# Optimization experiments

Hardware: AMD Instinct MI355X
Metric: run time of the kernel (lower is better)

Reference implementation:

```python
import jax, jax.numpy as jnp
import numpy as np

N, E, D = 50000, 1600000, 64


def setup_inputs() -> dict:
    key = jax.random.key(0)
    ks = jax.random.split(key, 10)
    s = 1.0 / np.sqrt(D)
    return {
        "x": jax.random.normal(ks[0], (N, D), dtype=jnp.float32),
        "edge_index": jax.random.randint(ks[1], (2, E), 0, N, dtype=jnp.int64),
        "edge_weight": jax.random.uniform(ks[2], (E,), dtype=jnp.float32),
        "W_rel1": jax.random.uniform(ks[3], (D, D), jnp.float32, -s, s),
        "b_rel1": jax.random.uniform(ks[4], (D,), jnp.float32, -s, s),
        "W_root1": jax.random.uniform(ks[5], (D, D), jnp.float32, -s, s),
        "W_rel2": jax.random.uniform(ks[6], (D, D), jnp.float32, -s, s),
        "b_rel2": jax.random.uniform(ks[7], (D,), jnp.float32, -s, s),
        "W_root2": jax.random.uniform(ks[8], (D, D), jnp.float32, -s, s),
    }


def graph_conv(x, src, dst, edge_weight, W_rel, b_rel, W_root):
    # message: edge_weight * x[src]; aggregate: sum into dst
    msg = edge_weight[:, None] * x[src]                      # [E, D]
    agg = jax.ops.segment_sum(msg, dst, num_segments=x.shape[0])  # [N, D]
    return agg @ W_rel.T + b_rel + x @ W_root.T


def reference(x, edge_index, edge_weight, W_rel1, b_rel1, W_root1, W_rel2, b_rel2, W_root2):
    src, dst = edge_index[0], edge_index[1]
    h = jax.nn.relu(graph_conv(x, src, dst, edge_weight, W_rel1, b_rel1, W_root1))
    # dropout is identity in eval mode
    h = jax.nn.relu(graph_conv(h, src, dst, edge_weight, W_rel2, b_rel2, W_root2))
    return h
```

## Files before the change

### kernel.cpp

```cpp
#include <hip/hip_runtime.h>


#define NN 50000
#define DD 64
#define EE 1600000
#define NPB 64
#define NB  ((NN + NPB - 1) / NPB)
#define PAD 2560
#define CHUNK 8192
#define NC ((EE + CHUNK - 1) / CHUNK)

static_assert(NC <= 256, "colscan_kernel scan width must cover all chunks");
static_assert(NB <= 1024, "LDS cursor arrays sized for NB");

typedef __attribute__((ext_vector_type(8))) short short8;
typedef __attribute__((ext_vector_type(4))) float f32x4;

__device__ __forceinline__ unsigned short f2bf(float f) {
    unsigned u = __float_as_uint(f);
    u += 0x7FFF + ((u >> 16) & 1);
    return (unsigned short)(u >> 16);
}
__device__ __forceinline__ float bflo(unsigned u) {
    return __uint_as_float(u << 16);
}
__device__ __forceinline__ float bfhi(unsigned u) {
    return __uint_as_float(u & 0xFFFF0000u);
}
__device__ __forceinline__ unsigned char f2fp8(float f) {
    unsigned p = __builtin_amdgcn_cvt_pk_fp8_f32(f, f, 0, false);
    return (unsigned char)(p & 0xFF);
}

#define XS_STR 72
#define WS_STR 72

template <typename TIn>
__device__ __forceinline__ void transform_body(
    int blk, int t,
    const TIn* __restrict__ xin,
    const float* __restrict__ Wrel, const float* __restrict__ Wroot,
    const float* __restrict__ bias,
    unsigned char* __restrict__ Z8, unsigned short* __restrict__ Yb,
    unsigned short* Xs, unsigned short* Ws)
{
    const int node0 = blk * 64;

#pragma unroll
    for (int i = 0; i < 8; ++i) {
        int flat = i * 256 + t;
        int row  = flat >> 4;
        int c4   = flat & 15;
        const float* src = (row < 64 ? Wrel + row * 64
                                     : Wroot + (row - 64) * 64) + c4 * 4;
        float4 v = *(const float4*)src;
        unsigned short* d = &Ws[row * WS_STR + c4 * 4];
        d[0] = f2bf(v.x); d[1] = f2bf(v.y); d[2] = f2bf(v.z); d[3] = f2bf(v.w);
    }
    if constexpr (sizeof(TIn) == 4) {
#pragma unroll
        for (int i = 0; i < 4; ++i) {
            int flat = i * 256 + t;
            int row  = flat >> 4;
            int c4   = flat & 15;
            int node = node0 + row;
            float4 v = make_float4(0.f, 0.f, 0.f, 0.f);
            if (node < NN) v = *(const float4*)((const float*)xin + (size_t)node * 64 + c4 * 4);
            unsigned short* d = &Xs[row * XS_STR + c4 * 4];
            d[0] = f2bf(v.x); d[1] = f2bf(v.y); d[2] = f2bf(v.z); d[3] = f2bf(v.w);
        }
    } else {
#pragma unroll
        for (int i = 0; i < 2; ++i) {
            int flat = i * 256 + t;
            int row  = flat >> 3;
            int c8   = flat & 7;
            int node = node0 + row;
            short8 v = {0,0,0,0,0,0,0,0};
            if (node < NN)
                v = *(const short8*)((const unsigned short*)xin + (size_t)node * 64 + c8 * 8);
            *(short8*)&Xs[row * XS_STR + c8 * 8] = v;
        }
    }
    __syncthreads();

    const int w    = t >> 6;
    const int lane = t & 63;
    const int l15  = lane & 15;
    const int quad = lane >> 4;

    short8 a0 = *(const short8*)&Xs[(w * 16 + l15) * XS_STR + quad * 8];
    short8 a1 = *(const short8*)&Xs[(w * 16 + l15) * XS_STR + 32 + quad * 8];

#pragma unroll
    for (int f = 0; f < 8; ++f) {
        short8 b0 = *(const short8*)&Ws[(f * 16 + l15) * WS_STR + quad * 8];
        short8 b1 = *(const short8*)&Ws[(f * 16 + l15) * WS_STR + 32 + quad * 8];
        f32x4 acc = {0.f, 0.f, 0.f, 0.f};
        acc = __builtin_amdgcn_mfma_f32_16x16x32_bf16(a0, b0, acc, 0, 0, 0);
        acc = __builtin_amdgcn_mfma_f32_16x16x32_bf16(a1, b1, acc, 0, 0, 0);
        const int col = f * 16 + l15;
#pragma unroll
        for (int r = 0; r < 4; ++r) {
            int node = node0 + w * 16 + quad * 4 + r;
            if (node < NN) {
                if (col < 64) Z8[(size_t)node * 64 + col] = f2fp8(acc[r]);
                else          Yb[(size_t)node * 64 + (col - 64)] =
                                  f2bf(acc[r] + bias[col - 64]);
            }
        }
    }
}

__global__ __launch_bounds__(256) void hist_t1_kernel(
    const int* __restrict__ ei, int* __restrict__ hist,
    const float* __restrict__ x,
    const float* __restrict__ Wrel, const float* __restrict__ Wroot,
    const float* __restrict__ bias,
    unsigned char* __restrict__ Z8, unsigned short* __restrict__ Yb)
{
    __shared__ int lh[NB];
    __shared__ unsigned short Xs[64 * XS_STR];
    __shared__ unsigned short Ws[128 * WS_STR];
    const int t = threadIdx.x;

    if (blockIdx.x < NC) {
        const int c = blockIdx.x;
        for (int b = t; b < NB; b += 256) lh[b] = 0;
        __syncthreads();
        const int base = c * CHUNK;
#pragma unroll 4
        for (int i = 0; i < CHUNK; i += 256) {
            int e = base + i + t;
            if (e < EE) atomicAdd(&lh[ei[EE + e] >> 6], 1);
        }
        __syncthreads();
        for (int b = t; b < NB; b += 256) hist[c * NB + b] = lh[b];
    } else {
        transform_body<float>(blockIdx.x - NC, t, x, Wrel, Wroot, bias,
                              Z8, Yb, Xs, Ws);
    }
}

__global__ __launch_bounds__(256) void transform2_kernel(
    const unsigned short* __restrict__ xin,
    const float* __restrict__ Wrel, const float* __restrict__ Wroot,
    const float* __restrict__ bias,
    unsigned char* __restrict__ Z8, unsigned short* __restrict__ Yb)
{
    __shared__ unsigned short Xs[64 * XS_STR];
    __shared__ unsigned short Ws[128 * WS_STR];
    transform_body<unsigned short>(blockIdx.x, threadIdx.x, xin, Wrel, Wroot,
                                   bias, Xs == nullptr ? Z8 : Z8, Yb, Xs, Ws);
}

__global__ __launch_bounds__(256) void colscan_kernel(
    const int* __restrict__ hist, int* __restrict__ offs, int* __restrict__ bsz)
{
    __shared__ int part[256];
    const int b = blockIdx.x, t = threadIdx.x;
    int h = (t < NC) ? hist[t * NB + b] : 0;
    part[t] = h;
    __syncthreads();
    for (int off = 1; off < 256; off <<= 1) {
        int v = (t >= off) ? part[t - off] : 0;
        __syncthreads();
        part[t] += v;
        __syncthreads();
    }
    if (t < NC) offs[t * NB + b] = b * PAD + (part[t] - h);
    if (t == 255) bsz[b] = part[255];
}

__global__ __launch_bounds__(256) void bin_kernel(
    const int* __restrict__ ei, const float* __restrict__ ew,
    const int* __restrict__ offs, unsigned* __restrict__ epk)
{
    __shared__ int cur[NB];
    const int c = blockIdx.x, t = threadIdx.x;
    for (int b = t; b < NB; b += 256) cur[b] = offs[c * NB + b];
    __syncthreads();
    const int base = c * CHUNK;
    for (int i = 0; i < CHUNK; i += 256) {
        int e = base + i + t;
        if (e < EE) {
            int src = ei[e];
            int dst = ei[EE + e];
            unsigned q = (unsigned)fmaf(ew[e], 1023.0f, 0.5f);
            int pos = atomicAdd(&cur[dst >> 6], 1);
            epk[pos] = (unsigned)src | ((unsigned)(dst & 63) << 16) | (q << 22);
        }
    }
}

template <bool FP32OUT>
__global__ __launch_bounds__(512) void aggregate_kernel(
    const unsigned* __restrict__ Z1,
    const uint2* __restrict__ Y4,
    const int* __restrict__ bsz,
    const unsigned* __restrict__ epk, void* __restrict__ Hout)
{
    __shared__ int      cnt[NPB];
    __shared__ int      nbeg[NPB];
    __shared__ int      cur[NPB];
    __shared__ unsigned stage[PAD];
    const int bk = blockIdx.x, t = threadIdx.x;
    const int base = bk * PAD;
    int sz = bsz[bk];
    if (sz > PAD) sz = PAD;

    if (t < NPB) cnt[t] = 0;
    __syncthreads();
    for (int i = t; i < sz; i += 512)
        atomicAdd(&cnt[(epk[base + i] >> 16) & 63], 1);
    __syncthreads();

    if (t < 64) {
        int c = cnt[t];
        int v = c;
        for (int off = 1; off < 64; off <<= 1) {
            int u = __shfl_up(v, off);
            if (t >= off) v += u;
        }
        nbeg[t] = v - c;
        cur[t]  = v - c;
    }
    __syncthreads();

    for (int i = t; i < sz; i += 512) {
        unsigned p = epk[base + i];
        int pos = atomicAdd(&cur[(p >> 16) & 63], 1);
        float w = (float)(p >> 22) * (1.0f / 1023.0f);
        stage[pos] = (p & 0xFFFFu) | ((unsigned)f2bf(w) << 16);
    }
    __syncthreads();

    const int lane = t & 63;
    const int wv   = t >> 6;
    const int s = lane & 15;
    const int q = lane >> 4;

#pragma unroll
    for (int k = 0; k < 8; ++k) {
        const int n6   = wv * 8 + k;
        const int node = bk * 64 + n6;
        const int b = nbeg[n6];
        const int e = b + cnt[n6];

        float a0 = 0.f, a1 = 0.f, a2 = 0.f, a3 = 0.f;
        int i = b;
        for (; i + 16 <= e; i += 16) {
            unsigned pA = stage[i + q];
            unsigned pB = stage[i + 4 + q];
            unsigned pC = stage[i + 8 + q];
            unsigned pD = stage[i + 12 + q];
            unsigned zA = Z1[(pA & 0xFFFF) * 16 + s];
            unsigned zB = Z1[(pB & 0xFFFF) * 16 + s];
            unsigned zC = Z1[(pC & 0xFFFF) * 16 + s];
            unsigned zD = Z1[(pD & 0xFFFF) * 16 + s];
            float wA = __uint_as_float(pA & 0xFFFF0000u);
            float wB = __uint_as_float(pB & 0xFFFF0000u);
            float wC = __uint_as_float(pC & 0xFFFF0000u);
            float wD = __uint_as_float(pD & 0xFFFF0000u);
            a0 = fmaf(wA, __builtin_amdgcn_cvt_f32_fp8(zA, 0), a0);
            a1 = fmaf(wA, __builtin_amdgcn_cvt_f32_fp8(zA, 1), a1);
            a2 = fmaf(wA, __builtin_amdgcn_cvt_f32_fp8(zA, 2), a2);
            a3 = fmaf(wA, __builtin_amdgcn_cvt_f32_fp8(zA, 3), a3);
            a0 = fmaf(wB, __builtin_amdgcn_cvt_f32_fp8(zB, 0), a0);
            a1 = fmaf(wB, __builtin_amdgcn_cvt_f32_fp8(zB, 1), a1);
            a2 = fmaf(wB, __builtin_amdgcn_cvt_f32_fp8(zB, 2), a2);
            a3 = fmaf(wB, __builtin_amdgcn_cvt_f32_fp8(zB, 3), a3);
            a0 = fmaf(wC, __builtin_amdgcn_cvt_f32_fp8(zC, 0), a0);
            a1 = fmaf(wC, __builtin_amdgcn_cvt_f32_fp8(zC, 1), a1);
            a2 = fmaf(wC, __builtin_amdgcn_cvt_f32_fp8(zC, 2), a2);
            a3 = fmaf(wC, __builtin_amdgcn_cvt_f32_fp8(zC, 3), a3);
            a0 = fmaf(wD, __builtin_amdgcn_cvt_f32_fp8(zD, 0), a0);
            a1 = fmaf(wD, __builtin_amdgcn_cvt_f32_fp8(zD, 1), a1);
            a2 = fmaf(wD, __builtin_amdgcn_cvt_f32_fp8(zD, 2), a2);
            a3 = fmaf(wD, __builtin_amdgcn_cvt_f32_fp8(zD, 3), a3);
        }
        for (; i < e; i += 4) {
            int ee = i + q;
            unsigned p = (ee < e) ? stage[ee] : 0u;
            unsigned z = Z1[(p & 0xFFFF) * 16 + s];
            float w = __uint_as_float(p & 0xFFFF0000u);
            a0 = fmaf(w, __builtin_amdgcn_cvt_f32_fp8(z, 0), a0);
            a1 = fmaf(w, __builtin_amdgcn_cvt_f32_fp8(z, 1), a1);
            a2 = fmaf(w, __builtin_amdgcn_cvt_f32_fp8(z, 2), a2);
            a3 = fmaf(w, __builtin_amdgcn_cvt_f32_fp8(z, 3), a3);
        }

        a0 += __shfl_xor(a0, 16); a0 += __shfl_xor(a0, 32);
        a1 += __shfl_xor(a1, 16); a1 += __shfl_xor(a1, 32);
        a2 += __shfl_xor(a2, 16); a2 += __shfl_xor(a2, 32);
        a3 += __shfl_xor(a3, 16); a3 += __shfl_xor(a3, 32);

        if (q == 0 && node < NN) {
            const uint2 y4 = Y4[node * 16 + s];
            float r0 = fmaxf(a0 + bflo(y4.x), 0.0f);
            float r1 = fmaxf(a1 + bfhi(y4.x), 0.0f);
            float r2 = fmaxf(a2 + bflo(y4.y), 0.0f);
            float r3 = fmaxf(a3 + bfhi(y4.y), 0.0f);
            if (FP32OUT) {
                ((float4*)Hout)[node * 16 + s] = make_float4(r0, r1, r2, r3);
            } else {
                uint2 o;
                o.x = (unsigned)f2bf(r0) | ((unsigned)f2bf(r1) << 16);
                o.y = (unsigned)f2bf(r2) | ((unsigned)f2bf(r3) << 16);
                ((uint2*)Hout)[node * 16 + s] = o;
            }
        }
    }
}

extern "C" void kernel_launch(void* const* d_in, const int* in_sizes, int n_in,
                              void* d_out, int out_size, void* d_ws, size_t ws_size,
                              hipStream_t stream)
{
    const float* x     = (const float*)d_in[0];
    const int*   ei    = (const int*)  d_in[1];
    const float* ew    = (const float*)d_in[2];
    const float* Wrel1 = (const float*)d_in[3];
    const float* brel1 = (const float*)d_in[4];
    const float* Wroot1= (const float*)d_in[5];
    const float* Wrel2 = (const float*)d_in[6];
    const float* brel2 = (const float*)d_in[7];
    const float* Wroot2= (const float*)d_in[8];

    float* out = (float*)d_out;

    const size_t ND = (size_t)NN * DD;
    char* w = (char*)d_ws;
    unsigned char*  Z8 = (unsigned char*)w;
    unsigned short* Yb = (unsigned short*)(w + ND);
    unsigned short* Hb = (unsigned short*)(w + ND * 3);
    unsigned* epk = (unsigned*)(w + ND * 5);
    int* bsz  = (int*)(w + ND * 5 + (size_t)NB * PAD * 4);
    int* hist = bsz + NB;
    int* offs = hist + (size_t)NC * NB;

    const int tb = (NN + 63) / 64;

    hist_t1_kernel<<<NC + tb, 256, 0, stream>>>(ei, hist, x, Wrel1, Wroot1,
                                                brel1, Z8, Yb);
    colscan_kernel<<<NB, 256, 0, stream>>>(hist, offs, bsz);
    bin_kernel    <<<NC, 256, 0, stream>>>(ei, ew, offs, epk);

    aggregate_kernel<false><<<NB, 512, 0, stream>>>(
        (const unsigned*)Z8, (const uint2*)Yb, bsz, epk, Hb);

    transform2_kernel<<<tb, 256, 0, stream>>>(Hb, Wrel2, Wroot2, brel2, Z8, Yb);
    aggregate_kernel<true><<<NB, 512, 0, stream>>>(
        (const unsigned*)Z8, (const uint2*)Yb, bsz, epk, out);
}
```

Before: 199.0 us.

## Persist sorted CSR edges from first aggregation and reuse in second layer

The first aggregation kernel now writes its LDS-sorted, per-node-grouped edge list back to global memory along with per-node begin/end offsets. The second aggregation becomes a simple CSR kernel, one wavefront per node, that reads the pre-sorted edges directly. This skips the second pass's LDS histogram, prefix scan and scatter sort. The cost is an extra global write of the edge array in layer one, and smaller blocks with less cross-node LDS staging in layer two.

```diff
diff --git a/kernel.cpp b/kernel.cpp
--- a/kernel.cpp
+++ b/kernel.cpp
@@ -151,7 +151,7 @@
     __shared__ unsigned short Xs[64 * XS_STR];
     __shared__ unsigned short Ws[128 * WS_STR];
     transform_body<unsigned short>(blockIdx.x, threadIdx.x, xin, Wrel, Wroot,
-                                   bias, Xs == nullptr ? Z8 : Z8, Yb, Xs, Ws);
+                                   bias, Z8, Yb, Xs, Ws);
 }
 
 __global__ __launch_bounds__(256) void colscan_kernel(
@@ -193,12 +193,13 @@
     }
 }
 
-template <bool FP32OUT>
-__global__ __launch_bounds__(512) void aggregate_kernel(
+__global__ __launch_bounds__(512) void aggregate_sort_kernel(
     const unsigned* __restrict__ Z1,
     const uint2* __restrict__ Y4,
     const int* __restrict__ bsz,
-    const unsigned* __restrict__ epk, void* __restrict__ Hout)
+    unsigned* __restrict__ epk,
+    int* __restrict__ beg, int* __restrict__ endo,
+    void* __restrict__ Hout)
 {
     __shared__ int      cnt[NPB];
     __shared__ int      nbeg[NPB];
@@ -222,8 +223,11 @@
             int u = __shfl_up(v, off);
             if (t >= off) v += u;
         }
-        nbeg[t] = v - c;
-        cur[t]  = v - c;
+        int ex = v - c;
+        nbeg[t] = ex;
+        cur[t]  = ex;
+        int g = bk * NPB + t;
+        if (g < NN) { beg[g] = base + ex; endo[g] = base + ex + c; }
     }
     __syncthreads();
 
@@ -234,6 +238,9 @@
         stage[pos] = (p & 0xFFFFu) | ((unsigned)f2bf(w) << 16);
     }
     __syncthreads();
+
+    for (int i = t; i < sz; i += 512)
+        epk[base + i] = stage[i];
 
     const int lane = t & 63;
     const int wv   = t >> 6;
@@ -301,15 +308,84 @@
             float r1 = fmaxf(a1 + bfhi(y4.x), 0.0f);
             float r2 = fmaxf(a2 + bflo(y4.y), 0.0f);
             float r3 = fmaxf(a3 + bfhi(y4.y), 0.0f);
-            if (FP32OUT) {
-                ((float4*)Hout)[node * 16 + s] = make_float4(r0, r1, r2, r3);
-            } else {
-                uint2 o;
-                o.x = (unsigned)f2bf(r0) | ((unsigned)f2bf(r1) << 16);
-                o.y = (unsigned)f2bf(r2) | ((unsigned)f2bf(r3) << 16);
-                ((uint2*)Hout)[node * 16 + s] = o;
-            }
-        }
+            uint2 o;
+            o.x = (unsigned)f2bf(r0) | ((unsigned)f2bf(r1) << 16);
+            o.y = (unsigned)f2bf(r2) | ((unsigned)f2bf(r3) << 16);
+            ((uint2*)Hout)[node * 16 + s] = o;
+        }
+    }
+}
+
+__global__ __launch_bounds__(256) void aggregate2_kernel(
+    const unsigned* __restrict__ Z1,
+    const uint2* __restrict__ Y4,
+    const int* __restrict__ beg, const int* __restrict__ endo,
+    const unsigned* __restrict__ epk, float4* __restrict__ Hout)
+{
+    const int lane = threadIdx.x & 63;
+    const int node = blockIdx.x * 4 + (threadIdx.x >> 6);
+    if (node >= NN) return;
+    const int s = lane & 15;
+    const int q = lane >> 4;
+
+    const int b = beg[node];
+    const int e = endo[node];
+    const uint2 y4 = Y4[node * 16 + s];
+
+    float a0 = 0.f, a1 = 0.f, a2 = 0.f, a3 = 0.f;
+    int i = b;
+    for (; i + 16 <= e; i += 16) {
+        unsigned pA = epk[i + q];
+        unsigned pB = epk[i + 4 + q];
+        unsigned pC = epk[i + 8 + q];
+        unsigned pD = epk[i + 12 + q];
+        unsigned zA = Z1[(pA & 0xFFFF) * 16 + s];
+        unsigned zB = Z1[(pB & 0xFFFF) * 16 + s];
+        unsigned zC = Z1[(pC & 0xFFFF) * 16 + s];
+        unsigned zD = Z1[(pD & 0xFFFF) * 16 + s];
+        float wA = __uint_as_float(pA & 0xFFFF0000u);
+        float wB = __uint_as_float(pB & 0xFFFF0000u);
+        float wC = __uint_as_float(pC & 0xFFFF0000u);
+        float wD = __uint_as_float(pD & 0xFFFF0000u);
+        a0 = fmaf(wA, __builtin_amdgcn_cvt_f32_fp8(zA, 0), a0);
+        a1 = fmaf(wA, __builtin_amdgcn_cvt_f32_fp8(zA, 1), a1);
+        a2 = fmaf(wA, __builtin_amdgcn_cvt_f32_fp8(zA, 2), a2);
+        a3 = fmaf(wA, __builtin_amdgcn_cvt_f32_fp8(zA, 3), a3);
+        a0 = fmaf(wB, __builtin_amdgcn_cvt_f32_fp8(zB, 0), a0);
+        a1 = fmaf(wB, __builtin_amdgcn_cvt_f32_fp8(zB, 1), a1);
+        a2 = fmaf(wB, __builtin_amdgcn_cvt_f32_fp8(zB, 2), a2);
+        a3 = fmaf(wB, __builtin_amdgcn_cvt_f32_fp8(zB, 3), a3);
+        a0 = fmaf(wC, __builtin_amdgcn_cvt_f32_fp8(zC, 0), a0);
+        a1 = fmaf(wC, __builtin_amdgcn_cvt_f32_fp8(zC, 1), a1);
+        a2 = fmaf(wC, __builtin_amdgcn_cvt_f32_fp8(zC, 2), a2);
+        a3 = fmaf(wC, __builtin_amdgcn_cvt_f32_fp8(zC, 3), a3);
+        a0 = fmaf(wD, __builtin_amdgcn_cvt_f32_fp8(zD, 0), a0);
+        a1 = fmaf(wD, __builtin_amdgcn_cvt_f32_fp8(zD, 1), a1);
+        a2 = fmaf(wD, __builtin_amdgcn_cvt_f32_fp8(zD, 2), a2);
+        a3 = fmaf(wD, __builtin_amdgcn_cvt_f32_fp8(zD, 3), a3);
+    }
+    for (; i < e; i += 4) {
+        int ee = i + q;
+        unsigned p = (ee < e) ? epk[ee] : 0u;
+        unsigned z = Z1[(p & 0xFFFF) * 16 + s];
+        float w = __uint_as_float(p & 0xFFFF0000u);
+        a0 = fmaf(w, __builtin_amdgcn_cvt_f32_fp8(z, 0), a0);
+        a1 = fmaf(w, __builtin_amdgcn_cvt_f32_fp8(z, 1), a1);
+        a2 = fmaf(w, __builtin_amdgcn_cvt_f32_fp8(z, 2), a2);
+        a3 = fmaf(w, __builtin_amdgcn_cvt_f32_fp8(z, 3), a3);
+    }
+
+    a0 += __shfl_xor(a0, 16); a0 += __shfl_xor(a0, 32);
+    a1 += __shfl_xor(a1, 16); a1 += __shfl_xor(a1, 32);
+    a2 += __shfl_xor(a2, 16); a2 += __shfl_xor(a2, 32);
+    a3 += __shfl_xor(a3, 16); a3 += __shfl_xor(a3, 32);
+
+    if (q == 0) {
+        float r0 = fmaxf(a0 + bflo(y4.x), 0.0f);
+        float r1 = fmaxf(a1 + bfhi(y4.x), 0.0f);
+        float r2 = fmaxf(a2 + bflo(y4.y), 0.0f);
+        float r3 = fmaxf(a3 + bfhi(y4.y), 0.0f);
+        Hout[node * 16 + s] = make_float4(r0, r1, r2, r3);
     }
 }
 
@@ -338,18 +414,21 @@
     int* bsz  = (int*)(w + ND * 5 + (size_t)NB * PAD * 4);
     int* hist = bsz + NB;
     int* offs = hist + (size_t)NC * NB;
+    int* beg  = offs + (size_t)NC * NB;
+    int* endo = beg + NN;
 
     const int tb = (NN + 63) / 64;
+    const int ab = (NN + 3) / 4;
 
     hist_t1_kernel<<<NC + tb, 256, 0, stream>>>(ei, hist, x, Wrel1, Wroot1,
                                                 brel1, Z8, Yb);
     colscan_kernel<<<NB, 256, 0, stream>>>(hist, offs, bsz);
     bin_kernel    <<<NC, 256, 0, stream>>>(ei, ew, offs, epk);
 
-    aggregate_kernel<false><<<NB, 512, 0, stream>>>(
-        (const unsigned*)Z8, (const uint2*)Yb, bsz, epk, Hb);
+    aggregate_sort_kernel<<<NB, 512, 0, stream>>>(
+        (const unsigned*)Z8, (const uint2*)Yb, bsz, epk, beg, endo, Hb);
 
     transform2_kernel<<<tb, 256, 0, stream>>>(Hb, Wrel2, Wroot2, brel2, Z8, Yb);
-    aggregate_kernel<true><<<NB, 512, 0, stream>>>(
-        (const unsigned*)Z8, (const uint2*)Yb, bsz, epk, out);
-}
+    aggregate2_kernel<<<ab, 256, 0, stream>>>(
+        (const unsigned*)Z8, (const uint2*)Yb, beg, endo, epk, (float4*)out);
+}
```

After: 195.6 us. No clear change (-1.7%).
